# Optimization experiments

Hardware: AMD Instinct MI355X
Metric: run time of the kernel (lower is better)

The kernel has to match this reference:

```python
import jax, jax.numpy as jnp
import numpy as np

DIM = 2048
N_HEADS = 32
N_KV_HEADS = 8
HEAD_DIM = DIM // N_HEADS  # 64
N_REP = N_HEADS // N_KV_HEADS  # 4
B, S = 2, 2048
MASK_VAL = -32768.0


def setup_inputs() -> dict:
    key = jax.random.key(0)
    ks = jax.random.split(key, 7)
    x = jax.random.normal(ks[0], (B, S, DIM), dtype=jnp.float32)
    freqs_cos = jax.random.uniform(ks[1], (S, HEAD_DIM // 2), dtype=jnp.float32)
    freqs_sin = jax.random.uniform(ks[2], (S, HEAD_DIM // 2), dtype=jnp.float32)
    sc = 1.0 / np.sqrt(DIM)
    wq = jax.random.normal(ks[3], (N_HEADS * HEAD_DIM, DIM), dtype=jnp.float32) * sc
    wk = jax.random.normal(ks[4], (N_KV_HEADS * HEAD_DIM, DIM), dtype=jnp.float32) * sc
    wv = jax.random.normal(ks[5], (N_KV_HEADS * HEAD_DIM, DIM), dtype=jnp.float32) * sc
    wo = jax.random.normal(ks[6], (DIM, N_HEADS * HEAD_DIM), dtype=jnp.float32) * sc
    return {"x": x, "freqs_cos": freqs_cos, "freqs_sin": freqs_sin,
            "wq": wq, "wk": wk, "wv": wv, "wo": wo}


def _apply_rope(q, k, cos, sin):
    # q: [B,S,H,D], k: [B,S,Hkv,D]; interleaved real/imag pairs in last dim
    def rot(t):
        tr = t.reshape(t.shape[:-1] + (-1, 2))  # [..., D/2, 2]
        t_r, t_i = tr[..., 0], tr[..., 1]
        c = cos[None, :, None, :]  # broadcast over batch and heads
        s = sin[None, :, None, :]
        o_r = t_r * c - t_i * s
        o_i = t_r * s + t_i * c
        return jnp.stack([o_r, o_i], axis=-1).reshape(t.shape)
    return rot(q), rot(k)


def reference(x, freqs_cos, freqs_sin, wq, wk, wv, wo):
    bsz, seqlen, _ = x.shape
    xq = (x @ wq.T).reshape(bsz, seqlen, N_HEADS, HEAD_DIM)
    xk = (x @ wk.T).reshape(bsz, seqlen, N_KV_HEADS, HEAD_DIM)
    xv = (x @ wv.T).reshape(bsz, seqlen, N_KV_HEADS, HEAD_DIM)
    xq, xk = _apply_rope(xq, xk, freqs_cos, freqs_sin)
    # GQA: repeat each kv head n_rep times contiguously (matches per-head cat loop)
    xk = jnp.repeat(xk, N_REP, axis=2)  # [B,S,H,D]
    xv = jnp.repeat(xv, N_REP, axis=2)
    # [B,H,S,D]
    q = xq.transpose(0, 2, 1, 3)
    k = xk.transpose(0, 2, 1, 3)
    v = xv.transpose(0, 2, 1, 3)
    scores = jnp.einsum('bhqd,bhkd->bhqk', q, k) / jnp.sqrt(jnp.float32(HEAD_DIM))
    causal = jnp.triu(jnp.full((seqlen, seqlen), MASK_VAL, dtype=scores.dtype), k=1)
    scores = scores + causal[None, None, :, :]
    probs = jax.nn.softmax(scores.astype(jnp.float32), axis=-1).astype(q.dtype)
    out = jnp.einsum('bhqk,bhkd->bhqd', probs, v)
    out = out.transpose(0, 2, 1, 3).reshape(bsz, seqlen, -1)
    return out @ wo.T
```

## Files before the change

kernel.cpp:

```cpp
#include <hip/hip_runtime.h>
#include <hip/hip_bf16.h>
#include <type_traits>

typedef __bf16 bf16;
typedef __bf16 bf16x2 __attribute__((ext_vector_type(2)));
typedef __bf16 bf16x4 __attribute__((ext_vector_type(4)));
typedef __bf16 bf16x8 __attribute__((ext_vector_type(8)));
typedef float f32x4 __attribute__((ext_vector_type(4)));

#define AS1 __attribute__((address_space(1)))
#define AS3 __attribute__((address_space(3)))

#define KAPPA 0.180336880111f

__device__ __forceinline__ void load_lds16(const void* g, void* l) {
  __builtin_amdgcn_global_load_lds((AS1 void*)g, (AS3 void*)l, 16, 0, 0);
}
__device__ __forceinline__ float exp2_fast(float x) {
  return __builtin_amdgcn_exp2f(x);
}

__global__ void f2b_all(const float* __restrict__ x, const float* __restrict__ wq,
                        const float* __restrict__ wk, const float* __restrict__ wv,
                        const float* __restrict__ wo, bf16* __restrict__ xb,
                        bf16* __restrict__ wqkv, bf16* __restrict__ wob) {
  int bid = blockIdx.x;
  const float* src;
  bf16* dst;
  int off;
  if (bid < 8192) { src = x; dst = xb; off = bid; }
  else if (bid < 12288) { src = wq; dst = wqkv; off = bid - 8192; }
  else if (bid < 13312) { src = wk; dst = wqkv + 4194304; off = bid - 12288; }
  else if (bid < 14336) { src = wv; dst = wqkv + 5242880; off = bid - 13312; }
  else { src = wo; dst = wob; off = bid - 14336; }
  int i = (off * 256 + threadIdx.x) * 4;
  float4 v = *(const float4*)(src + i);
  bf16x4 o = {(bf16)v.x, (bf16)v.y, (bf16)v.z, (bf16)v.w};
  *(bf16x4*)(dst + i) = o;
}

__global__ __launch_bounds__(256) void gemm_qkv(const bf16* __restrict__ A,
                                                const bf16* __restrict__ Bw,
                                                const float* __restrict__ fc,
                                                const float* __restrict__ fs,
                                                bf16* __restrict__ Qro,
                                                bf16* __restrict__ Kro,
                                                bf16* __restrict__ Vt) {
  const int K = 2048;
  __shared__ bf16 As[128][64];
  __shared__ bf16 Bs[128][64];
  const int t = threadIdx.x;
  const int wave = t >> 6, lane = t & 63, qd = lane >> 4, ln = lane & 15;
  const int wm = (wave >> 1) * 64;
  const int wn = (wave & 1) * 64;
  const int bn = blockIdx.x;
  const size_t bm = (size_t)blockIdx.y * 128;

  const bf16* Ab = A + bm * (size_t)K;
  const bf16* Bb = Bw + (size_t)bn * 128 * K;

  f32x4 acc[4][4] = {};

  for (int k0 = 0; k0 < K; k0 += 64) {
#pragma unroll
    for (int i = 0; i < 4; i++) {
      int e = i * 256 + t;
      int ro = e >> 3, gs = (e & 7) ^ (ro & 7);
      load_lds16(Ab + (size_t)ro * K + k0 + gs * 8,
                 (char*)As + i * 4096 + wave * 1024);
      load_lds16(Bb + (size_t)ro * K + k0 + gs * 8,
                 (char*)Bs + i * 4096 + wave * 1024);
    }
    __syncthreads();

#pragma unroll
    for (int kk = 0; kk < 2; kk++) {
      bf16x8 af[4], bfr[4];
#pragma unroll
      for (int i = 0; i < 4; i++) {
        int row = wm + i * 16 + ln;
        int ps = (kk * 4 + qd) ^ (row & 7);
        af[i] = *(const bf16x8*)((const char*)As + row * 128 + ps * 16);
      }
#pragma unroll
      for (int j = 0; j < 4; j++) {
        int row = wn + j * 16 + ln;
        int ps = (kk * 4 + qd) ^ (row & 7);
        bfr[j] = *(const bf16x8*)((const char*)Bs + row * 128 + ps * 16);
      }
#pragma unroll
      for (int i = 0; i < 4; i++)
#pragma unroll
        for (int j = 0; j < 4; j++)
          acc[i][j] = __builtin_amdgcn_mfma_f32_16x16x32_bf16(af[i], bfr[j],
                                                              acc[i][j], 0, 0, 0);
    }
    __syncthreads();
  }

  const int b = (int)(bm >> 11);
  const int sb = (int)(bm & 2047) + wm;
  const bool odd = ln & 1;

  if (bn < 20) {
    const bool isQ = bn < 16;
    const float kap = isQ ? KAPPA : 1.0f;
    const int hh = isQ ? (bn * 2 + (wn >> 6)) : ((bn - 16) * 2 + (wn >> 6));
    bf16* dst = isQ ? (Qro + ((size_t)(b * 32 + hh) * 2048) * 64)
                    : (Kro + ((size_t)(b * 8 + hh) * 2048) * 64);
#pragma unroll
    for (int i = 0; i < 4; i++) {
#pragma unroll
      for (int j = 0; j < 4; j++) {
        const int d = j * 16 + ln;
        const int i_f = d >> 1;
#pragma unroll
        for (int r = 0; r < 4; r++) {
          int s = sb + i * 16 + qd * 4 + r;
          float v = acc[i][j][r];
          float p = __shfl_xor(v, 1);
          float cv = fc[s * 32 + i_f] * kap;
          float sv = fs[s * 32 + i_f] * kap;
          float o = odd ? (p * sv + v * cv) : (v * cv - p * sv);
          dst[(size_t)s * 64 + d] = (bf16)o;
        }
      }
    }
  } else {
    const int kh = (bn - 20) * 2 + (wn >> 6);
#pragma unroll
    for (int i = 0; i < 4; i++)
#pragma unroll
      for (int j = 0; j < 4; j++) {
        const int d = j * 16 + ln;
        int s = sb + i * 16 + qd * 4;
        bf16x4 ov = {(bf16)acc[i][j][0], (bf16)acc[i][j][1],
                     (bf16)acc[i][j][2], (bf16)acc[i][j][3]};
        *(bf16x4*)&Vt[((size_t)(b * 8 + kh) * 64 + d) * 2048 + s] = ov;
      }
  }
}

template <typename OutT>
__global__ __launch_bounds__(256, 4) void gemm_bt64(const bf16* __restrict__ A,
                                                    const bf16* __restrict__ Bw,
                                                    OutT* __restrict__ C,
                                                    int M, int N, int K) {
  __shared__ bf16 As[64][64];
  __shared__ bf16 Bs[128][64];
  const int t = threadIdx.x;
  const int wave = t >> 6, lane = t & 63, qd = lane >> 4, ln = lane & 15;
  const int wm = (wave >> 1) * 32;
  const int wn = (wave & 1) * 64;
  const size_t bm = (size_t)blockIdx.y * 64;
  const size_t bn = (size_t)blockIdx.x * 128;

  const bf16* Ab = A + bm * (size_t)K;
  const bf16* Bb = Bw + bn * (size_t)K;

  f32x4 acc[2][4] = {};

  for (int k0 = 0; k0 < K; k0 += 64) {
#pragma unroll
    for (int i = 0; i < 2; i++) {
      int e = i * 256 + t;
      int ro = e >> 3, gs = (e & 7) ^ (ro & 7);
      load_lds16(Ab + (size_t)ro * K + k0 + gs * 8,
                 (char*)As + i * 4096 + wave * 1024);
    }
#pragma unroll
    for (int i = 0; i < 4; i++) {
      int e = i * 256 + t;
      int ro = e >> 3, gs = (e & 7) ^ (ro & 7);
      load_lds16(Bb + (size_t)ro * K + k0 + gs * 8,
                 (char*)Bs + i * 4096 + wave * 1024);
    }
    __syncthreads();

#pragma unroll
    for (int kk = 0; kk < 2; kk++) {
      bf16x8 af[2], bfr[4];
#pragma unroll
      for (int i = 0; i < 2; i++) {
        int row = wm + i * 16 + ln;
        int ps = (kk * 4 + qd) ^ (row & 7);
        af[i] = *(const bf16x8*)((const char*)As + row * 128 + ps * 16);
      }
#pragma unroll
      for (int j = 0; j < 4; j++) {
        int row = wn + j * 16 + ln;
        int ps = (kk * 4 + qd) ^ (row & 7);
        bfr[j] = *(const bf16x8*)((const char*)Bs + row * 128 + ps * 16);
      }
#pragma unroll
      for (int i = 0; i < 2; i++)
#pragma unroll
        for (int j = 0; j < 4; j++)
          acc[i][j] = __builtin_amdgcn_mfma_f32_16x16x32_bf16(af[i], bfr[j],
                                                              acc[i][j], 0, 0, 0);
    }
    __syncthreads();
  }

#pragma unroll
  for (int i = 0; i < 2; i++)
#pragma unroll
    for (int j = 0; j < 4; j++)
#pragma unroll
      for (int r = 0; r < 4; r++) {
        size_t row = bm + wm + i * 16 + qd * 4 + r;
        size_t col = bn + wn + j * 16 + ln;
        C[row * N + col] = (OutT)acc[i][j][r];
      }
}

__global__ __launch_bounds__(256, 3) void attn_fwd(const bf16* __restrict__ Q,
                                                   const bf16* __restrict__ Kg,
                                                   const bf16* __restrict__ Vg,
                                                   bf16* __restrict__ O) {
  __shared__ bf16 Qs[128][64];
  __shared__ bf16 Ks[64][64];
  __shared__ bf16 Vs[64][64];
  __shared__ bf16 Ps[128][64];
  const int t = threadIdx.x;
  const int wave = t >> 6, lane = t & 63, qd = lane >> 4, ln = lane & 15;
  const int bid = blockIdx.x;
  const int qt = 15 - (bid >> 6);
  const int bh = bid & 63;
  const int b = bh >> 5, h = bh & 31, kh = h >> 2;
  const bf16* Qb = Q + ((size_t)(b * 32 + h) * 2048 + qt * 128) * 64;
  const bf16* Kb = Kg + (size_t)(b * 8 + kh) * 2048 * 64;
  const bf16* Vb = Vg + (size_t)(b * 8 + kh) * 64 * 2048;
  char* PsB = (char*)Ps;

#pragma unroll
  for (int i = 0; i < 4; i++) {
    int e = i * 256 + t;
    int row = e >> 3, sg = (e & 7) ^ (row & 7);
    load_lds16(Qb + (size_t)row * 64 + sg * 8, (char*)Qs + i * 4096 + wave * 1024);
  }

  f32x4 o_acc[4][2] = {};
  float l_st[2] = {0.f, 0.f};
  const int q0 = qt * 128 + wave * 32;
  const int nkb = 2 * qt + 2;

  for (int kb = 0; kb < nkb; kb++) {
    __syncthreads();
#pragma unroll
    for (int i = 0; i < 2; i++) {
      int e = i * 256 + t;
      int row = e >> 3, sg = (e & 7) ^ (row & 7);
      load_lds16(Kb + (size_t)(kb * 64 + row) * 64 + sg * 8,
                 (char*)Ks + i * 4096 + wave * 1024);
      load_lds16(Vb + (size_t)row * 2048 + kb * 64 + sg * 8,
                 (char*)Vs + i * 4096 + wave * 1024);
    }
    __syncthreads();

    f32x4 s_acc[4][2] = {};
#pragma unroll
    for (int kk = 0; kk < 2; kk++) {
      bf16x8 ak[4], bq[2];
#pragma unroll
      for (int j = 0; j < 4; j++) {
        int row = j * 16 + ln;
        int ph = (kk * 4 + qd) ^ (ln & 7);
        ak[j] = *(const bf16x8*)((const char*)Ks + row * 128 + ph * 16);
      }
#pragma unroll
      for (int mi = 0; mi < 2; mi++) {
        int row = wave * 32 + mi * 16 + ln;
        int ph = (kk * 4 + qd) ^ (ln & 7);
        bq[mi] = *(const bf16x8*)((const char*)Qs + row * 128 + ph * 16);
      }
#pragma unroll
      for (int j = 0; j < 4; j++)
#pragma unroll
        for (int mi = 0; mi < 2; mi++)
          s_acc[j][mi] = __builtin_amdgcn_mfma_f32_16x16x32_bf16(
              ak[j], bq[mi], s_acc[j][mi], 0, 0, 0);
    }

    auto smax = [&](auto maskc) {
      constexpr bool MASK = decltype(maskc)::value;
#pragma unroll
      for (int mi = 0; mi < 2; mi++) {
        const int qv = q0 + mi * 16 + ln;
        const int prow = wave * 32 + mi * 16 + ln;
        float rs = 0.f;
#pragma unroll
        for (int j = 0; j < 4; j++) {
          bf16x4 pk;
#pragma unroll
          for (int r = 0; r < 4; r++) {
            float s = s_acc[j][mi][r];
            if (MASK) {
              int k_glob = kb * 64 + j * 16 + qd * 4 + r;
              if (k_glob > qv) s = -1e5f;
            }
            float pv = exp2_fast(s - 16.f);
            rs += pv;
            pk[r] = (bf16)pv;
          }
          int ps = (j * 2 + (qd >> 1)) ^ (ln & 7);
          *(bf16x4*)(PsB + prow * 128 + ps * 16 + (qd & 1) * 8) = pk;
        }
        l_st[mi] += rs;
      }
    };
    if (kb * 64 + 63 > q0) smax(std::true_type{});
    else smax(std::false_type{});

#pragma unroll
    for (int kk = 0; kk < 2; kk++) {
      bf16x8 av[4], bp[2];
#pragma unroll
      for (int dj = 0; dj < 4; dj++) {
        int row = dj * 16 + ln;
        int ph = (kk * 4 + qd) ^ (ln & 7);
        av[dj] = *(const bf16x8*)((const char*)Vs + row * 128 + ph * 16);
      }
#pragma unroll
      for (int mi = 0; mi < 2; mi++) {
        int prow = wave * 32 + mi * 16 + ln;
        int ph = (kk * 4 + qd) ^ (ln & 7);
        bp[mi] = *(const bf16x8*)(PsB + prow * 128 + ph * 16);
      }
#pragma unroll
      for (int dj = 0; dj < 4; dj++)
#pragma unroll
        for (int mi = 0; mi < 2; mi++)
          o_acc[dj][mi] = __builtin_amdgcn_mfma_f32_16x16x32_bf16(
              av[dj], bp[mi], o_acc[dj][mi], 0, 0, 0);
    }
  }

#pragma unroll
  for (int mi = 0; mi < 2; mi++) {
    float lt = l_st[mi];
    lt += __shfl_xor(lt, 16);
    lt += __shfl_xor(lt, 32);
    float inv = 1.f / lt;
    int q_idx = qt * 128 + wave * 32 + mi * 16 + ln;
#pragma unroll
    for (int dj = 0; dj < 4; dj++) {
      bf16x4 ov;
#pragma unroll
      for (int r = 0; r < 4; r++) ov[r] = (bf16)(o_acc[dj][mi][r] * inv);
      *(bf16x4*)&O[((size_t)(b * 2048 + q_idx) * 32 + h) * 64 + dj * 16 + qd * 4] = ov;
    }
  }
}

extern "C" void kernel_launch(void* const* d_in, const int* in_sizes, int n_in,
                              void* d_out, int out_size, void* d_ws,
                              size_t ws_size, hipStream_t stream) {
  const float* x = (const float*)d_in[0];
  const float* fc = (const float*)d_in[1];
  const float* fs = (const float*)d_in[2];
  const float* wq = (const float*)d_in[3];
  const float* wk = (const float*)d_in[4];
  const float* wv = (const float*)d_in[5];
  const float* wo = (const float*)d_in[6];
  float* out = (float*)d_out;

  char* ws = (char*)d_ws;
  const size_t MB = (size_t)1 << 20;
  bf16* xb   = (bf16*)(ws + 0 * MB);
  bf16* wqkv = (bf16*)(ws + 16 * MB);
  bf16* wob  = (bf16*)(ws + 28 * MB);
  bf16* Qro  = (bf16*)(ws + 36 * MB);
  bf16* Kro  = (bf16*)(ws + 52 * MB);
  bf16* Vt   = (bf16*)(ws + 56 * MB);
  bf16* Oa   = (bf16*)(ws + 60 * MB);

  dim3 blk(256);
  f2b_all<<<18432, blk, 0, stream>>>(x, wq, wk, wv, wo, xb, wqkv, wob);
  gemm_qkv<<<dim3(24, 32), blk, 0, stream>>>(xb, wqkv, fc, fs, Qro, Kro, Vt);
  attn_fwd<<<1024, blk, 0, stream>>>(Qro, Kro, Vt, Oa);
  gemm_bt64<float><<<dim3(16, 64), blk, 0, stream>>>(Oa, wob, out, 4096, 2048, 2048);
}
```

Measured before the change: 306.6 us.

## Enlarge attention query tile to 256 and split-K the output projection

Attention now processes 256 query rows per block (64 per wave), with Q fragments held in registers across all KV blocks. This cuts K/V reloads per query and removes repeated Q LDS reads, at the cost of fewer blocks, more LDS and registers, and occupancy lowered to 2. The output projection now uses 128x128 tiles with a 2-way split-K that accumulates into the zeroed output via float atomics. That needs an extra memset and adds atomic traffic and nondeterministic summation order.

```diff
diff --git a/kernel.cpp b/kernel.cpp
--- a/kernel.cpp
+++ b/kernel.cpp
@@ -141,37 +141,32 @@
   }
 }
 
-template <typename OutT>
-__global__ __launch_bounds__(256, 4) void gemm_bt64(const bf16* __restrict__ A,
-                                                    const bf16* __restrict__ Bw,
-                                                    OutT* __restrict__ C,
-                                                    int M, int N, int K) {
-  __shared__ bf16 As[64][64];
+__global__ __launch_bounds__(256) void gemm_out_sk(const bf16* __restrict__ A,
+                                                   const bf16* __restrict__ Bw,
+                                                   float* __restrict__ C) {
+  const int K = 2048;
+  __shared__ bf16 As[128][64];
   __shared__ bf16 Bs[128][64];
   const int t = threadIdx.x;
   const int wave = t >> 6, lane = t & 63, qd = lane >> 4, ln = lane & 15;
-  const int wm = (wave >> 1) * 32;
+  const int wm = (wave >> 1) * 64;
   const int wn = (wave & 1) * 64;
-  const size_t bm = (size_t)blockIdx.y * 64;
+  const size_t bm = (size_t)blockIdx.y * 128;
   const size_t bn = (size_t)blockIdx.x * 128;
-
-  const bf16* Ab = A + bm * (size_t)K;
-  const bf16* Bb = Bw + bn * (size_t)K;
-
-  f32x4 acc[2][4] = {};
-
-  for (int k0 = 0; k0 < K; k0 += 64) {
-#pragma unroll
-    for (int i = 0; i < 2; i++) {
+  const int z = blockIdx.z;
+
+  const bf16* Ab = A + bm * (size_t)K + z * 1024;
+  const bf16* Bb = Bw + bn * (size_t)K + z * 1024;
+
+  f32x4 acc[4][4] = {};
+
+  for (int k0 = 0; k0 < 1024; k0 += 64) {
+#pragma unroll
+    for (int i = 0; i < 4; i++) {
       int e = i * 256 + t;
       int ro = e >> 3, gs = (e & 7) ^ (ro & 7);
       load_lds16(Ab + (size_t)ro * K + k0 + gs * 8,
                  (char*)As + i * 4096 + wave * 1024);
-    }
-#pragma unroll
-    for (int i = 0; i < 4; i++) {
-      int e = i * 256 + t;
-      int ro = e >> 3, gs = (e & 7) ^ (ro & 7);
       load_lds16(Bb + (size_t)ro * K + k0 + gs * 8,
                  (char*)Bs + i * 4096 + wave * 1024);
     }
@@ -179,9 +174,9 @@
 
 #pragma unroll
     for (int kk = 0; kk < 2; kk++) {
-      bf16x8 af[2], bfr[4];
-#pragma unroll
-      for (int i = 0; i < 2; i++) {
+      bf16x8 af[4], bfr[4];
+#pragma unroll
+      for (int i = 0; i < 4; i++) {
         int row = wm + i * 16 + ln;
         int ps = (kk * 4 + qd) ^ (row & 7);
         af[i] = *(const bf16x8*)((const char*)As + row * 128 + ps * 16);
@@ -193,7 +188,7 @@
         bfr[j] = *(const bf16x8*)((const char*)Bs + row * 128 + ps * 16);
       }
 #pragma unroll
-      for (int i = 0; i < 2; i++)
+      for (int i = 0; i < 4; i++)
 #pragma unroll
         for (int j = 0; j < 4; j++)
           acc[i][j] = __builtin_amdgcn_mfma_f32_16x16x32_bf16(af[i], bfr[j],
@@ -203,47 +198,48 @@
   }
 
 #pragma unroll
-  for (int i = 0; i < 2; i++)
+  for (int i = 0; i < 4; i++)
 #pragma unroll
     for (int j = 0; j < 4; j++)
 #pragma unroll
       for (int r = 0; r < 4; r++) {
         size_t row = bm + wm + i * 16 + qd * 4 + r;
         size_t col = bn + wn + j * 16 + ln;
-        C[row * N + col] = (OutT)acc[i][j][r];
-      }
-}
-
-__global__ __launch_bounds__(256, 3) void attn_fwd(const bf16* __restrict__ Q,
+        unsafeAtomicAdd(&C[row * 2048 + col], acc[i][j][r]);
+      }
+}
+
+__global__ __launch_bounds__(256, 2) void attn_fwd(const bf16* __restrict__ Q,
                                                    const bf16* __restrict__ Kg,
                                                    const bf16* __restrict__ Vg,
                                                    bf16* __restrict__ O) {
-  __shared__ bf16 Qs[128][64];
+  __shared__ bf16 Qs[256][64];
   __shared__ bf16 Ks[64][64];
   __shared__ bf16 Vs[64][64];
-  __shared__ bf16 Ps[128][64];
+  __shared__ bf16 Ps[256][64];
   const int t = threadIdx.x;
   const int wave = t >> 6, lane = t & 63, qd = lane >> 4, ln = lane & 15;
   const int bid = blockIdx.x;
-  const int qt = 15 - (bid >> 6);
+  const int qt = 7 - (bid >> 6);
   const int bh = bid & 63;
   const int b = bh >> 5, h = bh & 31, kh = h >> 2;
-  const bf16* Qb = Q + ((size_t)(b * 32 + h) * 2048 + qt * 128) * 64;
+  const bf16* Qb = Q + ((size_t)(b * 32 + h) * 2048 + qt * 256) * 64;
   const bf16* Kb = Kg + (size_t)(b * 8 + kh) * 2048 * 64;
   const bf16* Vb = Vg + (size_t)(b * 8 + kh) * 64 * 2048;
   char* PsB = (char*)Ps;
 
 #pragma unroll
-  for (int i = 0; i < 4; i++) {
+  for (int i = 0; i < 8; i++) {
     int e = i * 256 + t;
     int row = e >> 3, sg = (e & 7) ^ (row & 7);
     load_lds16(Qb + (size_t)row * 64 + sg * 8, (char*)Qs + i * 4096 + wave * 1024);
   }
 
-  f32x4 o_acc[4][2] = {};
-  float l_st[2] = {0.f, 0.f};
-  const int q0 = qt * 128 + wave * 32;
-  const int nkb = 2 * qt + 2;
+  f32x4 o_acc[4][4] = {};
+  float l_st[4] = {0.f, 0.f, 0.f, 0.f};
+  bf16x8 bq[4][2];
+  const int q0 = qt * 256 + wave * 64;
+  const int nkb = 4 * qt + 4;
 
   for (int kb = 0; kb < nkb; kb++) {
     __syncthreads();
@@ -258,10 +254,21 @@
     }
     __syncthreads();
 
-    f32x4 s_acc[4][2] = {};
+    if (kb == 0) {
+#pragma unroll
+      for (int mi = 0; mi < 4; mi++)
+#pragma unroll
+        for (int kk = 0; kk < 2; kk++) {
+          int row = wave * 64 + mi * 16 + ln;
+          int ph = (kk * 4 + qd) ^ (ln & 7);
+          bq[mi][kk] = *(const bf16x8*)((const char*)Qs + row * 128 + ph * 16);
+        }
+    }
+
+    f32x4 s_acc[4][4] = {};
 #pragma unroll
     for (int kk = 0; kk < 2; kk++) {
-      bf16x8 ak[4], bq[2];
+      bf16x8 ak[4];
 #pragma unroll
       for (int j = 0; j < 4; j++) {
         int row = j * 16 + ln;
@@ -269,25 +276,19 @@
         ak[j] = *(const bf16x8*)((const char*)Ks + row * 128 + ph * 16);
       }
 #pragma unroll
-      for (int mi = 0; mi < 2; mi++) {
-        int row = wave * 32 + mi * 16 + ln;
-        int ph = (kk * 4 + qd) ^ (ln & 7);
-        bq[mi] = *(const bf16x8*)((const char*)Qs + row * 128 + ph * 16);
-      }
-#pragma unroll
       for (int j = 0; j < 4; j++)
 #pragma unroll
-        for (int mi = 0; mi < 2; mi++)
+        for (int mi = 0; mi < 4; mi++)
           s_acc[j][mi] = __builtin_amdgcn_mfma_f32_16x16x32_bf16(
-              ak[j], bq[mi], s_acc[j][mi], 0, 0, 0);
+              ak[j], bq[mi][kk], s_acc[j][mi], 0, 0, 0);
     }
 
     auto smax = [&](auto maskc) {
       constexpr bool MASK = decltype(maskc)::value;
 #pragma unroll
-      for (int mi = 0; mi < 2; mi++) {
+      for (int mi = 0; mi < 4; mi++) {
         const int qv = q0 + mi * 16 + ln;
-        const int prow = wave * 32 + mi * 16 + ln;
+        const int prow = wave * 64 + mi * 16 + ln;
         float rs = 0.f;
 #pragma unroll
         for (int j = 0; j < 4; j++) {
@@ -314,7 +315,7 @@
 
 #pragma unroll
     for (int kk = 0; kk < 2; kk++) {
-      bf16x8 av[4], bp[2];
+      bf16x8 av[4], bp[4];
 #pragma unroll
       for (int dj = 0; dj < 4; dj++) {
         int row = dj * 16 + ln;
@@ -322,27 +323,27 @@
         av[dj] = *(const bf16x8*)((const char*)Vs + row * 128 + ph * 16);
       }
 #pragma unroll
-      for (int mi = 0; mi < 2; mi++) {
-        int prow = wave * 32 + mi * 16 + ln;
+      for (int mi = 0; mi < 4; mi++) {
+        int prow = wave * 64 + mi * 16 + ln;
         int ph = (kk * 4 + qd) ^ (ln & 7);
         bp[mi] = *(const bf16x8*)(PsB + prow * 128 + ph * 16);
       }
 #pragma unroll
       for (int dj = 0; dj < 4; dj++)
 #pragma unroll
-        for (int mi = 0; mi < 2; mi++)
+        for (int mi = 0; mi < 4; mi++)
           o_acc[dj][mi] = __builtin_amdgcn_mfma_f32_16x16x32_bf16(
               av[dj], bp[mi], o_acc[dj][mi], 0, 0, 0);
     }
   }
 
 #pragma unroll
-  for (int mi = 0; mi < 2; mi++) {
+  for (int mi = 0; mi < 4; mi++) {
     float lt = l_st[mi];
     lt += __shfl_xor(lt, 16);
     lt += __shfl_xor(lt, 32);
     float inv = 1.f / lt;
-    int q_idx = qt * 128 + wave * 32 + mi * 16 + ln;
+    int q_idx = qt * 256 + wave * 64 + mi * 16 + ln;
 #pragma unroll
     for (int dj = 0; dj < 4; dj++) {
       bf16x4 ov;
@@ -376,8 +377,9 @@
   bf16* Oa   = (bf16*)(ws + 60 * MB);
 
   dim3 blk(256);
+  hipMemsetAsync(out, 0, (size_t)4096 * 2048 * 4, stream);
   f2b_all<<<18432, blk, 0, stream>>>(x, wq, wk, wv, wo, xb, wqkv, wob);
   gemm_qkv<<<dim3(24, 32), blk, 0, stream>>>(xb, wqkv, fc, fs, Qro, Kro, Vt);
-  attn_fwd<<<1024, blk, 0, stream>>>(Qro, Kro, Vt, Oa);
-  gemm_bt64<float><<<dim3(16, 64), blk, 0, stream>>>(Oa, wob, out, 4096, 2048, 2048);
-}
+  attn_fwd<<<512, blk, 0, stream>>>(Qro, Kro, Vt, Oa);
+  gemm_out_sk<<<dim3(16, 32, 2), blk, 0, stream>>>(Oa, wob, out);
+}
```

After: 351.4 us. 14.6% more time.
